# Optimization experiments

Measured on AMD Instinct MI355X. Metric: run time of the kernel, lower is better.

## Reference

```python
import jax, jax.numpy as jnp
import numpy as np


def setup_inputs() -> dict:
    key = jax.random.key(0)
    ks = jax.random.split(key, 6)
    B, D, U = 65536, 256, 256
    L, T, Ep, Es = 2, 2, 2, 2
    s = 1.0 / np.sqrt(D)  # VarianceScaling-like scale
    return {
        "x": jax.random.normal(ks[0], (B, D), jnp.float32),
        "we_task": jax.random.normal(ks[1], (L, T * Ep, D, U), jnp.float32) * s,
        "be_task": jnp.zeros((L, T * Ep, U), jnp.float32),
        "we_share": jax.random.normal(ks[2], (L, Es, D, U), jnp.float32) * s,
        "be_share": jnp.zeros((L, Es, U), jnp.float32),
        "wg_task": jax.random.normal(ks[3], (L, T, D, Ep + Es), jnp.float32) * s,
        "bg_task": jnp.zeros((L, T, Ep + Es), jnp.float32),
        "wg_share": jax.random.normal(ks[4], (L - 1, D, T * Ep + Es), jnp.float32) * s,
        "bg_share": jnp.zeros((L - 1, T * Ep + Es), jnp.float32),
    }


def reference(x, we_task, be_task, we_share, be_share, wg_task, bg_task, wg_share, bg_share):
    L, TE, D, U = we_task.shape
    T = wg_task.shape[1]
    Ep = TE // T
    Es = we_share.shape[1]
    B = x.shape[0]
    # PLE: level 0 feeds the same input to every task slot and the shared slot
    ins = [x] * (T + 1)
    for lvl in range(L):
        last = lvl == L - 1
        xt = jnp.stack(ins[:T])  # [T,B,D] task-specific inputs
        wt = we_task[lvl].reshape(T, Ep, D, U)
        bt = be_task[lvl].reshape(T, Ep, U)
        # task experts, batched over tasks and experts: [T,B,Ep,U]
        e_task = jax.nn.relu(jnp.einsum('tbd,tedu->tbeu', xt, wt) + bt[:, None, :, :])
        # shared experts on the shared input: [B,Es,U]
        e_share = jax.nn.relu(jnp.einsum('bd,edu->beu', ins[-1], we_share[lvl]) + be_share[lvl][None])
        # per-task softmax gates: [T,B,Ep+Es]
        gates = jax.nn.softmax(jnp.einsum('tbd,tdg->tbg', xt, wg_task[lvl]) + bg_task[lvl][:, None, :], axis=-1)
        outs = []
        for t in range(T):
            experts = jnp.concatenate([e_task[t], e_share], axis=1)  # [B,Ep+Es,U]
            outs.append(jnp.einsum('beu,be->bu', experts, gates[t]))
        if not last:
            g_s = jax.nn.softmax(ins[-1] @ wg_share[lvl] + bg_share[lvl], axis=-1)  # [B,T*Ep+Es]
            all_e = jnp.concatenate(
                [e_task.transpose(1, 0, 2, 3).reshape(B, T * Ep, U), e_share], axis=1)
            outs.append(jnp.einsum('beu,be->bu', all_e, g_s))
        ins = outs
    return jnp.stack(ins)  # [T,B,U]
```

## Files before the change

### kernel.cpp

```cpp
#include <hip/hip_runtime.h>

typedef short s8v __attribute__((ext_vector_type(8)));
typedef float f4v __attribute__((ext_vector_type(4)));

#define NB 65536
#define BT 64
#define STR 264
#define PW_ELEMS 786432
#define PG0_OFF  786432
#define PG1T0_OFF 790528
#define PG1T1_OFF 794624
#define TOTAL_PACK 798720

__device__ __forceinline__ unsigned short f2bf(float f) {
  unsigned u = __float_as_uint(f);
  u += 0x7FFF + ((u >> 16) & 1);
  return (unsigned short)(u >> 16);
}

__global__ void pack_weights(const float* __restrict__ we_task,
                             const float* __restrict__ we_share,
                             const float* __restrict__ wg_task,
                             const float* __restrict__ wg_share,
                             unsigned short* __restrict__ ws) {
  int i = blockIdx.x * 256 + threadIdx.x;
  if (i >= TOTAL_PACK) return;
  float v = 0.f;
  if (i < PW_ELEMS) {
    int j = i & 7;
    int t = i >> 3;
    int lane = t & 63; t >>= 6;
    int kc = t & 7;    t >>= 3;
    int nt = t & 15;   t >>= 4;
    int lvl = t / 6, e = t % 6;
    int d = kc * 32 + (lane >> 4) * 8 + j;
    int u = nt * 16 + (lane & 15);
    if (e < 4) v = we_task[((lvl * 4 + e) * 256 + d) * 256 + u];
    else       v = we_share[((lvl * 2 + (e - 4)) * 256 + d) * 256 + u];
  } else {
    int gi = i - PW_ELEMS;
    int which = gi >> 12;
    int r = gi & 4095;
    int j = r & 7;
    int lane = (r >> 3) & 63;
    int kc = r >> 9;
    int d = kc * 32 + (lane >> 4) * 8 + j;
    int n = lane & 15;
    if (which == 0) {
      if (n < 4)       v = wg_task[0 * 1024 + d * 4 + n];
      else if (n < 8)  v = wg_task[1 * 1024 + d * 4 + (n - 4)];
      else if (n < 14) v = wg_share[d * 6 + (n - 8)];
    } else if (which == 1) {
      if (n < 4) v = wg_task[2 * 1024 + d * 4 + n];
    } else {
      if (n < 4) v = wg_task[3 * 1024 + d * 4 + n];
    }
  }
  ws[i] = f2bf(v);
}

__device__ __forceinline__ s8v ld_af(const unsigned short* Ab, int m, int kc,
                                     int col, int rq) {
  return *(const s8v*)&Ab[(m * 16 + col) * STR + kc * 32 + rq * 8];
}

__launch_bounds__(512, 2)
__global__ void ple_fused(const float* __restrict__ x,
                          const float* __restrict__ be_task,
                          const float* __restrict__ be_share,
                          const float* __restrict__ bg_task,
                          const float* __restrict__ bg_share,
                          const unsigned short* __restrict__ ws,
                          float* __restrict__ out) {
  __shared__ unsigned short A0[BT * STR];
  __shared__ unsigned short A1[2][BT * STR];
  __shared__ unsigned short A2[BT * STR];
  __shared__ float g_lds[BT * 16];
  __shared__ float bias_lds[6 * 256];

  const int tid  = threadIdx.x;
  const int lane = tid & 63;
  const int wave = tid >> 6;
  const int col  = lane & 15;
  const int rq   = lane >> 4;
  const int r0   = blockIdx.x * BT;

  {
    const float* xb = x + (long)r0 * 256;
#pragma unroll
    for (int i = 0; i < 8; ++i) {
      int f = tid + i * 512;
      int row = f >> 6, c4 = f & 63;
      const float4 v = *(const float4*)(xb + row * 256 + c4 * 4);
      unsigned lo = ((unsigned)f2bf(v.y) << 16) | f2bf(v.x);
      unsigned hi = ((unsigned)f2bf(v.w) << 16) | f2bf(v.z);
      *(uint2*)&A0[row * STR + c4 * 4] = make_uint2(lo, hi);
    }
    for (int idx = tid; idx < 1536; idx += 512)
      bias_lds[idx] = (idx < 1024) ? be_task[idx] : be_share[idx - 1024];
  }
  __syncthreads();

  if (wave < 4) {
    const int m = wave;
    f4v ag = {0.f, 0.f, 0.f, 0.f};
    for (int kc = 0; kc < 8; ++kc) {
      s8v af = ld_af(A0, m, kc, col, rq);
      s8v bg = *(const s8v*)&ws[PG0_OFF + (kc * 64 + lane) * 8];
      ag = __builtin_amdgcn_mfma_f32_16x16x32_bf16(af, bg, ag, 0, 0, 0);
    }
#pragma unroll
    for (int r = 0; r < 4; ++r)
      g_lds[(m * 16 + rq * 4 + r) * 16 + col] = ag[r];
  }
  __syncthreads();

  if (tid < 64) {
    float* g = &g_lds[tid * 16];
    {
      float a0 = g[0] + bg_task[0], a1 = g[1] + bg_task[1];
      float a2 = g[2] + bg_task[2], a3 = g[3] + bg_task[3];
      float mx = fmaxf(fmaxf(a0, a1), fmaxf(a2, a3));
      float e0 = __expf(a0 - mx), e1 = __expf(a1 - mx);
      float e2 = __expf(a2 - mx), e3 = __expf(a3 - mx);
      float inv = 1.f / (e0 + e1 + e2 + e3);
      g[0] = e0 * inv; g[1] = e1 * inv; g[2] = e2 * inv; g[3] = e3 * inv;
    }
    {
      float a0 = g[4] + bg_task[4], a1 = g[5] + bg_task[5];
      float a2 = g[6] + bg_task[6], a3 = g[7] + bg_task[7];
      float mx = fmaxf(fmaxf(a0, a1), fmaxf(a2, a3));
      float e0 = __expf(a0 - mx), e1 = __expf(a1 - mx);
      float e2 = __expf(a2 - mx), e3 = __expf(a3 - mx);
      float inv = 1.f / (e0 + e1 + e2 + e3);
      g[4] = e0 * inv; g[5] = e1 * inv; g[6] = e2 * inv; g[7] = e3 * inv;
    }
    {
      float a[6], mx = -1e30f;
#pragma unroll
      for (int k = 0; k < 6; ++k) { a[k] = g[8 + k] + bg_share[k]; mx = fmaxf(mx, a[k]); }
      float s = 0.f;
#pragma unroll
      for (int k = 0; k < 6; ++k) { a[k] = __expf(a[k] - mx); s += a[k]; }
      float inv = 1.f / s;
#pragma unroll
      for (int k = 0; k < 6; ++k) g[8 + k] = a[k] * inv;
    }
  }
  __syncthreads();

#pragma unroll
  for (int q = 0; q < 2; ++q) {
    const int nt = wave + q * 8;
    f4v acc[4][6];
#pragma unroll
    for (int m = 0; m < 4; ++m)
#pragma unroll
      for (int e = 0; e < 6; ++e) acc[m][e] = (f4v){0.f, 0.f, 0.f, 0.f};

    const unsigned short* pw = ws + nt * 4096;
    s8v bfc[6];
#pragma unroll
    for (int e = 0; e < 6; ++e)
      bfc[e] = *(const s8v*)&pw[e * 65536 + lane * 8];
#pragma unroll
    for (int kc = 0; kc < 8; ++kc) {
      s8v bfn[6];
      if (kc < 7) {
#pragma unroll
        for (int e = 0; e < 6; ++e)
          bfn[e] = *(const s8v*)&pw[e * 65536 + ((kc + 1) * 64 + lane) * 8];
      }
      s8v af[4];
#pragma unroll
      for (int m = 0; m < 4; ++m) af[m] = ld_af(A0, m, kc, col, rq);
#pragma unroll
      for (int m = 0; m < 4; ++m)
#pragma unroll
        for (int e = 0; e < 6; ++e)
          acc[m][e] = __builtin_amdgcn_mfma_f32_16x16x32_bf16(af[m], bfc[e], acc[m][e], 0, 0, 0);
#pragma unroll
      for (int e = 0; e < 6; ++e) bfc[e] = bfn[e];
    }

    const int u = nt * 16 + col;
    float bz[6];
#pragma unroll
    for (int e = 0; e < 6; ++e) bz[e] = bias_lds[e * 256 + u];
#pragma unroll
    for (int m = 0; m < 4; ++m) {
#pragma unroll
      for (int r = 0; r < 4; ++r) {
        int row = m * 16 + rq * 4 + r;
        const float* gr = &g_lds[row * 16];
        f4v ga = *(const f4v*)&gr[0];
        f4v gb = *(const f4v*)&gr[4];
        f4v gc = *(const f4v*)&gr[8];
        float gs4 = gr[12], gs5 = gr[13];
        float E0 = fmaxf(acc[m][0][r] + bz[0], 0.f);
        float E1 = fmaxf(acc[m][1][r] + bz[1], 0.f);
        float E2 = fmaxf(acc[m][2][r] + bz[2], 0.f);
        float E3 = fmaxf(acc[m][3][r] + bz[3], 0.f);
        float E4 = fmaxf(acc[m][4][r] + bz[4], 0.f);
        float E5 = fmaxf(acc[m][5][r] + bz[5], 0.f);
        float o0 = ga[0] * E0 + ga[1] * E1 + ga[2] * E4 + ga[3] * E5;
        float o1 = gb[0] * E2 + gb[1] * E3 + gb[2] * E4 + gb[3] * E5;
        float o2 = gc[0] * E0 + gc[1] * E1 + gc[2] * E2 + gc[3] * E3 + gs4 * E4 + gs5 * E5;
        A1[0][row * STR + u] = f2bf(o0);
        A1[1][row * STR + u] = f2bf(o1);
        A2[row * STR + u]    = f2bf(o2);
      }
    }
  }
  __syncthreads();

  for (int idx = tid; idx < 1536; idx += 512)
    bias_lds[idx] = (idx < 1024) ? be_task[1024 + idx] : be_share[512 + idx - 1024];

  {
    const int m = wave >> 1;
    const int t = wave & 1;
    const unsigned short* pg = ws + (t ? PG1T1_OFF : PG1T0_OFF);
    f4v ag = {0.f, 0.f, 0.f, 0.f};
    for (int kc = 0; kc < 8; ++kc) {
      s8v af = ld_af(A1[t], m, kc, col, rq);
      s8v bg = *(const s8v*)&pg[(kc * 64 + lane) * 8];
      ag = __builtin_amdgcn_mfma_f32_16x16x32_bf16(af, bg, ag, 0, 0, 0);
    }
    if (col < 4) {
#pragma unroll
      for (int r = 0; r < 4; ++r)
        g_lds[(m * 16 + rq * 4 + r) * 16 + t * 4 + col] = ag[r];
    }
  }
  __syncthreads();

  if (tid < 64) {
    float* g = &g_lds[tid * 16];
    {
      float a0 = g[0] + bg_task[8],  a1 = g[1] + bg_task[9];
      float a2 = g[2] + bg_task[10], a3 = g[3] + bg_task[11];
      float mx = fmaxf(fmaxf(a0, a1), fmaxf(a2, a3));
      float e0 = __expf(a0 - mx), e1 = __expf(a1 - mx);
      float e2 = __expf(a2 - mx), e3 = __expf(a3 - mx);
      float inv = 1.f / (e0 + e1 + e2 + e3);
      g[0] = e0 * inv; g[1] = e1 * inv; g[2] = e2 * inv; g[3] = e3 * inv;
    }
    {
      float a0 = g[4] + bg_task[12], a1 = g[5] + bg_task[13];
      float a2 = g[6] + bg_task[14], a3 = g[7] + bg_task[15];
      float mx = fmaxf(fmaxf(a0, a1), fmaxf(a2, a3));
      float e0 = __expf(a0 - mx), e1 = __expf(a1 - mx);
      float e2 = __expf(a2 - mx), e3 = __expf(a3 - mx);
      float inv = 1.f / (e0 + e1 + e2 + e3);
      g[4] = e0 * inv; g[5] = e1 * inv; g[6] = e2 * inv; g[7] = e3 * inv;
    }
  }
  __syncthreads();

#pragma unroll
  for (int q = 0; q < 2; ++q) {
    const int nt = wave + q * 8;
    f4v acc[4][6];
#pragma unroll
    for (int m = 0; m < 4; ++m)
#pragma unroll
      for (int e = 0; e < 6; ++e) acc[m][e] = (f4v){0.f, 0.f, 0.f, 0.f};

    const unsigned short* pw = ws + 6 * 65536 + nt * 4096;
    s8v bfc[6];
#pragma unroll
    for (int e = 0; e < 6; ++e)
      bfc[e] = *(const s8v*)&pw[e * 65536 + lane * 8];
#pragma unroll
    for (int kc = 0; kc < 8; ++kc) {
      s8v bfn[6];
      if (kc < 7) {
#pragma unroll
        for (int e = 0; e < 6; ++e)
          bfn[e] = *(const s8v*)&pw[e * 65536 + ((kc + 1) * 64 + lane) * 8];
      }
      s8v a0f[4], a1f[4], a2f[4];
#pragma unroll
      for (int m = 0; m < 4; ++m) {
        a0f[m] = ld_af(A1[0], m, kc, col, rq);
        a1f[m] = ld_af(A1[1], m, kc, col, rq);
        a2f[m] = ld_af(A2,    m, kc, col, rq);
      }
#pragma unroll
      for (int m = 0; m < 4; ++m) {
        acc[m][0] = __builtin_amdgcn_mfma_f32_16x16x32_bf16(a0f[m], bfc[0], acc[m][0], 0, 0, 0);
        acc[m][1] = __builtin_amdgcn_mfma_f32_16x16x32_bf16(a0f[m], bfc[1], acc[m][1], 0, 0, 0);
        acc[m][2] = __builtin_amdgcn_mfma_f32_16x16x32_bf16(a1f[m], bfc[2], acc[m][2], 0, 0, 0);
        acc[m][3] = __builtin_amdgcn_mfma_f32_16x16x32_bf16(a1f[m], bfc[3], acc[m][3], 0, 0, 0);
        acc[m][4] = __builtin_amdgcn_mfma_f32_16x16x32_bf16(a2f[m], bfc[4], acc[m][4], 0, 0, 0);
        acc[m][5] = __builtin_amdgcn_mfma_f32_16x16x32_bf16(a2f[m], bfc[5], acc[m][5], 0, 0, 0);
      }
#pragma unroll
      for (int e = 0; e < 6; ++e) bfc[e] = bfn[e];
    }

    const int u = nt * 16 + col;
    float bz[6];
#pragma unroll
    for (int e = 0; e < 6; ++e) bz[e] = bias_lds[e * 256 + u];
#pragma unroll
    for (int m = 0; m < 4; ++m) {
#pragma unroll
      for (int r = 0; r < 4; ++r) {
        int row = m * 16 + rq * 4 + r;
        const float* gr = &g_lds[row * 16];
        f4v ga = *(const f4v*)&gr[0];
        f4v gb = *(const f4v*)&gr[4];
        float E0 = fmaxf(acc[m][0][r] + bz[0], 0.f);
        float E1 = fmaxf(acc[m][1][r] + bz[1], 0.f);
        float E2 = fmaxf(acc[m][2][r] + bz[2], 0.f);
        float E3 = fmaxf(acc[m][3][r] + bz[3], 0.f);
        float E4 = fmaxf(acc[m][4][r] + bz[4], 0.f);
        float E5 = fmaxf(acc[m][5][r] + bz[5], 0.f);
        float o0 = ga[0] * E0 + ga[1] * E1 + ga[2] * E4 + ga[3] * E5;
        float o1 = gb[0] * E2 + gb[1] * E3 + gb[2] * E4 + gb[3] * E5;
        out[(long)(r0 + row) * 256 + u] = o0;
        out[16777216L + (long)(r0 + row) * 256 + u] = o1;
      }
    }
  }
}

extern "C" void kernel_launch(void* const* d_in, const int* in_sizes, int n_in,
                              void* d_out, int out_size, void* d_ws, size_t ws_size,
                              hipStream_t stream) {
  const float* x        = (const float*)d_in[0];
  const float* we_task  = (const float*)d_in[1];
  const float* be_task  = (const float*)d_in[2];
  const float* we_share = (const float*)d_in[3];
  const float* be_share = (const float*)d_in[4];
  const float* wg_task  = (const float*)d_in[5];
  const float* bg_task  = (const float*)d_in[6];
  const float* wg_share = (const float*)d_in[7];
  const float* bg_share = (const float*)d_in[8];
  unsigned short* ws = (unsigned short*)d_ws;
  float* out = (float*)d_out;

  hipLaunchKernelGGL(pack_weights, dim3((TOTAL_PACK + 255) / 256), dim3(256), 0, stream,
                     we_task, we_share, wg_task, wg_share, ws);
  hipLaunchKernelGGL(ple_fused, dim3(NB / BT), dim3(512), 0, stream,
                     x, be_task, be_share, bg_task, bg_share, ws, out);
}
```

Measured before the change: 369.2 us.

## Switch expert GEMMs to 32x32x16 MFMA with repacked weight layout

```diff
diff --git a/kernel.cpp b/kernel.cpp
--- a/kernel.cpp
+++ b/kernel.cpp
@@ -2,6 +2,7 @@
 
 typedef short s8v __attribute__((ext_vector_type(8)));
 typedef float f4v __attribute__((ext_vector_type(4)));
+typedef float f16v __attribute__((ext_vector_type(16)));
 
 #define NB 65536
 #define BT 64
@@ -30,11 +31,11 @@
     int j = i & 7;
     int t = i >> 3;
     int lane = t & 63; t >>= 6;
-    int kc = t & 7;    t >>= 3;
-    int nt = t & 15;   t >>= 4;
+    int ks = t & 15;   t >>= 4;
+    int nt = t & 7;    t >>= 3;
     int lvl = t / 6, e = t % 6;
-    int d = kc * 32 + (lane >> 4) * 8 + j;
-    int u = nt * 16 + (lane & 15);
+    int d = ks * 16 + (lane >> 5) * 8 + j;
+    int u = nt * 32 + (lane & 31);
     if (e < 4) v = we_task[((lvl * 4 + e) * 256 + d) * 256 + u];
     else       v = we_share[((lvl * 2 + (e - 4)) * 256 + d) * 256 + u];
   } else {
@@ -59,9 +60,14 @@
   ws[i] = f2bf(v);
 }
 
-__device__ __forceinline__ s8v ld_af(const unsigned short* Ab, int m, int kc,
-                                     int col, int rq) {
+__device__ __forceinline__ s8v ld_a16(const unsigned short* Ab, int m, int kc,
+                                      int col, int rq) {
   return *(const s8v*)&Ab[(m * 16 + col) * STR + kc * 32 + rq * 8];
+}
+
+__device__ __forceinline__ s8v ld_a32(const unsigned short* Ab, int m, int ks,
+                                      int lane) {
+  return *(const s8v*)&Ab[(m * 32 + (lane & 31)) * STR + ks * 16 + (lane >> 5) * 8];
 }
 
 __launch_bounds__(512, 2)
@@ -83,6 +89,7 @@
   const int wave = tid >> 6;
   const int col  = lane & 15;
   const int rq   = lane >> 4;
+  const int hi   = lane >> 5;
   const int r0   = blockIdx.x * BT;
 
   {
@@ -93,8 +100,8 @@
       int row = f >> 6, c4 = f & 63;
       const float4 v = *(const float4*)(xb + row * 256 + c4 * 4);
       unsigned lo = ((unsigned)f2bf(v.y) << 16) | f2bf(v.x);
-      unsigned hi = ((unsigned)f2bf(v.w) << 16) | f2bf(v.z);
-      *(uint2*)&A0[row * STR + c4 * 4] = make_uint2(lo, hi);
+      unsigned hi2 = ((unsigned)f2bf(v.w) << 16) | f2bf(v.z);
+      *(uint2*)&A0[row * STR + c4 * 4] = make_uint2(lo, hi2);
     }
     for (int idx = tid; idx < 1536; idx += 512)
       bias_lds[idx] = (idx < 1024) ? be_task[idx] : be_share[idx - 1024];
@@ -105,7 +112,7 @@
     const int m = wave;
     f4v ag = {0.f, 0.f, 0.f, 0.f};
     for (int kc = 0; kc < 8; ++kc) {
-      s8v af = ld_af(A0, m, kc, col, rq);
+      s8v af = ld_a16(A0, m, kc, col, rq);
       s8v bg = *(const s8v*)&ws[PG0_OFF + (kc * 64 + lane) * 8];
       ag = __builtin_amdgcn_mfma_f32_16x16x32_bf16(af, bg, ag, 0, 0, 0);
     }
@@ -149,60 +156,53 @@
   }
   __syncthreads();
 
-#pragma unroll
-  for (int q = 0; q < 2; ++q) {
-    const int nt = wave + q * 8;
-    f4v acc[4][6];
-#pragma unroll
-    for (int m = 0; m < 4; ++m)
-#pragma unroll
-      for (int e = 0; e < 6; ++e) acc[m][e] = (f4v){0.f, 0.f, 0.f, 0.f};
-
-    const unsigned short* pw = ws + nt * 4096;
-    s8v bfc[6];
-#pragma unroll
-    for (int e = 0; e < 6; ++e)
-      bfc[e] = *(const s8v*)&pw[e * 65536 + lane * 8];
-#pragma unroll
-    for (int kc = 0; kc < 8; ++kc) {
-      s8v bfn[6];
-      if (kc < 7) {
+  {
+    const int nt = wave;
+    const int u  = nt * 32 + (lane & 31);
+    float bz[6];
+#pragma unroll
+    for (int e = 0; e < 6; ++e) bz[e] = bias_lds[e * 256 + u];
+
+#pragma unroll
+    for (int mp = 0; mp < 2; ++mp) {
+      f16v acc[6];
+#pragma unroll
+      for (int e = 0; e < 6; ++e) acc[e] = (f16v)(0.f);
+
+      s8v bfc[6];
+#pragma unroll
+      for (int e = 0; e < 6; ++e)
+        bfc[e] = *(const s8v*)&ws[(((e << 3) + nt) << 13) + lane * 8];
+#pragma unroll
+      for (int ks = 0; ks < 16; ++ks) {
+        s8v bfn[6];
+        if (ks < 15) {
+#pragma unroll
+          for (int e = 0; e < 6; ++e)
+            bfn[e] = *(const s8v*)&ws[(((e << 3) + nt) << 13) + (ks + 1) * 512 + lane * 8];
+        }
+        s8v af = ld_a32(A0, mp, ks, lane);
 #pragma unroll
         for (int e = 0; e < 6; ++e)
-          bfn[e] = *(const s8v*)&pw[e * 65536 + ((kc + 1) * 64 + lane) * 8];
+          acc[e] = __builtin_amdgcn_mfma_f32_32x32x16_bf16(af, bfc[e], acc[e], 0, 0, 0);
+#pragma unroll
+        for (int e = 0; e < 6; ++e) bfc[e] = bfn[e];
       }
-      s8v af[4];
-#pragma unroll
-      for (int m = 0; m < 4; ++m) af[m] = ld_af(A0, m, kc, col, rq);
-#pragma unroll
-      for (int m = 0; m < 4; ++m)
-#pragma unroll
-        for (int e = 0; e < 6; ++e)
-          acc[m][e] = __builtin_amdgcn_mfma_f32_16x16x32_bf16(af[m], bfc[e], acc[m][e], 0, 0, 0);
-#pragma unroll
-      for (int e = 0; e < 6; ++e) bfc[e] = bfn[e];
-    }
-
-    const int u = nt * 16 + col;
-    float bz[6];
-#pragma unroll
-    for (int e = 0; e < 6; ++e) bz[e] = bias_lds[e * 256 + u];
-#pragma unroll
-    for (int m = 0; m < 4; ++m) {
-#pragma unroll
-      for (int r = 0; r < 4; ++r) {
-        int row = m * 16 + rq * 4 + r;
+
+#pragma unroll
+      for (int r = 0; r < 16; ++r) {
+        int row = mp * 32 + (r & 3) + 8 * (r >> 2) + 4 * hi;
         const float* gr = &g_lds[row * 16];
         f4v ga = *(const f4v*)&gr[0];
         f4v gb = *(const f4v*)&gr[4];
         f4v gc = *(const f4v*)&gr[8];
         float gs4 = gr[12], gs5 = gr[13];
-        float E0 = fmaxf(acc[m][0][r] + bz[0], 0.f);
-        float E1 = fmaxf(acc[m][1][r] + bz[1], 0.f);
-        float E2 = fmaxf(acc[m][2][r] + bz[2], 0.f);
-        float E3 = fmaxf(acc[m][3][r] + bz[3], 0.f);
-        float E4 = fmaxf(acc[m][4][r] + bz[4], 0.f);
-        float E5 = fmaxf(acc[m][5][r] + bz[5], 0.f);
+        float E0 = fmaxf(acc[0][r] + bz[0], 0.f);
+        float E1 = fmaxf(acc[1][r] + bz[1], 0.f);
+        float E2 = fmaxf(acc[2][r] + bz[2], 0.f);
+        float E3 = fmaxf(acc[3][r] + bz[3], 0.f);
+        float E4 = fmaxf(acc[4][r] + bz[4], 0.f);
+        float E5 = fmaxf(acc[5][r] + bz[5], 0.f);
         float o0 = ga[0] * E0 + ga[1] * E1 + ga[2] * E4 + ga[3] * E5;
         float o1 = gb[0] * E2 + gb[1] * E3 + gb[2] * E4 + gb[3] * E5;
         float o2 = gc[0] * E0 + gc[1] * E1 + gc[2] * E2 + gc[3] * E3 + gs4 * E4 + gs5 * E5;
@@ -223,7 +223,7 @@
     const unsigned short* pg = ws + (t ? PG1T1_OFF : PG1T0_OFF);
     f4v ag = {0.f, 0.f, 0.f, 0.f};
     for (int kc = 0; kc < 8; ++kc) {
-      s8v af = ld_af(A1[t], m, kc, col, rq);
+      s8v af = ld_a16(A1[t], m, kc, col, rq);
       s8v bg = *(const s8v*)&pg[(kc * 64 + lane) * 8];
       ag = __builtin_amdgcn_mfma_f32_16x16x32_bf16(af, bg, ag, 0, 0, 0);
     }
@@ -258,66 +258,57 @@
   }
   __syncthreads();
 
-#pragma unroll
-  for (int q = 0; q < 2; ++q) {
-    const int nt = wave + q * 8;
-    f4v acc[4][6];
-#pragma unroll
-    for (int m = 0; m < 4; ++m)
-#pragma unroll
-      for (int e = 0; e < 6; ++e) acc[m][e] = (f4v){0.f, 0.f, 0.f, 0.f};
-
-    const unsigned short* pw = ws + 6 * 65536 + nt * 4096;
-    s8v bfc[6];
-#pragma unroll
-    for (int e = 0; e < 6; ++e)
-      bfc[e] = *(const s8v*)&pw[e * 65536 + lane * 8];
-#pragma unroll
-    for (int kc = 0; kc < 8; ++kc) {
-      s8v bfn[6];
-      if (kc < 7) {
-#pragma unroll
-        for (int e = 0; e < 6; ++e)
-          bfn[e] = *(const s8v*)&pw[e * 65536 + ((kc + 1) * 64 + lane) * 8];
+  {
+    const int nt = wave;
+    const int u  = nt * 32 + (lane & 31);
+    float bz[6];
+#pragma unroll
+    for (int e = 0; e < 6; ++e) bz[e] = bias_lds[e * 256 + u];
+
+#pragma unroll
+    for (int mp = 0; mp < 2; ++mp) {
+      f16v acc[6];
+#pragma unroll
+      for (int e = 0; e < 6; ++e) acc[e] = (f16v)(0.f);
+
+      const int l1b = 6 * 8 * 8192;
+      s8v bfc[6];
+#pragma unroll
+      for (int e = 0; e < 6; ++e)
+        bfc[e] = *(const s8v*)&ws[l1b + (((e << 3) + nt) << 13) + lane * 8];
+#pragma unroll
+      for (int ks = 0; ks < 16; ++ks) {
+        s8v bfn[6];
+        if (ks < 15) {
+#pragma unroll
+          for (int e = 0; e < 6; ++e)
+            bfn[e] = *(const s8v*)&ws[l1b + (((e << 3) + nt) << 13) + (ks + 1) * 512 + lane * 8];
+        }
+        s8v a0f = ld_a32(A1[0], mp, ks, lane);
+        s8v a1f = ld_a32(A1[1], mp, ks, lane);
+        s8v a2f = ld_a32(A2,    mp, ks, lane);
+        acc[0] = __builtin_amdgcn_mfma_f32_32x32x16_bf16(a0f, bfc[0], acc[0], 0, 0, 0);
+        acc[1] = __builtin_amdgcn_mfma_f32_32x32x16_bf16(a0f, bfc[1], acc[1], 0, 0, 0);
+        acc[2] = __builtin_amdgcn_mfma_f32_32x32x16_bf16(a1f, bfc[2], acc[2], 0, 0, 0);
+        acc[3] = __builtin_amdgcn_mfma_f32_32x32x16_bf16(a1f, bfc[3], acc[3], 0, 0, 0);
+        acc[4] = __builtin_amdgcn_mfma_f32_32x32x16_bf16(a2f, bfc[4], acc[4], 0, 0, 0);
+        acc[5] = __builtin_amdgcn_mfma_f32_32x32x16_bf16(a2f, bfc[5], acc[5], 0, 0, 0);
+#pragma unroll
+        for (int e = 0; e < 6; ++e) bfc[e] = bfn[e];
       }
-      s8v a0f[4], a1f[4], a2f[4];
-#pragma unroll
-      for (int m = 0; m < 4; ++m) {
-        a0f[m] = ld_af(A1[0], m, kc, col, rq);
-        a1f[m] = ld_af(A1[1], m, kc, col, rq);
-        a2f[m] = ld_af(A2,    m, kc, col, rq);
-      }
-#pragma unroll
-      for (int m = 0; m < 4; ++m) {
-        acc[m][0] = __builtin_amdgcn_mfma_f32_16x16x32_bf16(a0f[m], bfc[0], acc[m][0], 0, 0, 0);
-        acc[m][1] = __builtin_amdgcn_mfma_f32_16x16x32_bf16(a0f[m], bfc[1], acc[m][1], 0, 0, 0);
-        acc[m][2] = __builtin_amdgcn_mfma_f32_16x16x32_bf16(a1f[m], bfc[2], acc[m][2], 0, 0, 0);
-        acc[m][3] = __builtin_amdgcn_mfma_f32_16x16x32_bf16(a1f[m], bfc[3], acc[m][3], 0, 0, 0);
-        acc[m][4] = __builtin_amdgcn_mfma_f32_16x16x32_bf16(a2f[m], bfc[4], acc[m][4], 0, 0, 0);
-        acc[m][5] = __builtin_amdgcn_mfma_f32_16x16x32_bf16(a2f[m], bfc[5], acc[m][5], 0, 0, 0);
-      }
-#pragma unroll
-      for (int e = 0; e < 6; ++e) bfc[e] = bfn[e];
-    }
-
-    const int u = nt * 16 + col;
-    float bz[6];
-#pragma unroll
-    for (int e = 0; e < 6; ++e) bz[e] = bias_lds[e * 256 + u];
-#pragma unroll
-    for (int m = 0; m < 4; ++m) {
-#pragma unroll
-      for (int r = 0; r < 4; ++r) {
-        int row = m * 16 + rq * 4 + r;
+
+#pragma unroll
+      for (int r = 0; r < 16; ++r) {
+        int row = mp * 32 + (r & 3) + 8 * (r >> 2) + 4 * hi;
         const float* gr = &g_lds[row * 16];
         f4v ga = *(const f4v*)&gr[0];
         f4v gb = *(const f4v*)&gr[4];
-        float E0 = fmaxf(acc[m][0][r] + bz[0], 0.f);
-        float E1 = fmaxf(acc[m][1][r] + bz[1], 0.f);
-        float E2 = fmaxf(acc[m][2][r] + bz[2], 0.f);
-        float E3 = fmaxf(acc[m][3][r] + bz[3], 0.f);
-        float E4 = fmaxf(acc[m][4][r] + bz[4], 0.f);
-        float E5 = fmaxf(acc[m][5][r] + bz[5], 0.f);
+        float E0 = fmaxf(acc[0][r] + bz[0], 0.f);
+        float E1 = fmaxf(acc[1][r] + bz[1], 0.f);
+        float E2 = fmaxf(acc[2][r] + bz[2], 0.f);
+        float E3 = fmaxf(acc[3][r] + bz[3], 0.f);
+        float E4 = fmaxf(acc[4][r] + bz[4], 0.f);
+        float E5 = fmaxf(acc[5][r] + bz[5], 0.f);
         float o0 = ga[0] * E0 + ga[1] * E1 + ga[2] * E4 + ga[3] * E5;
         float o1 = gb[0] * E2 + gb[1] * E3 + gb[2] * E4 + gb[3] * E5;
         out[(long)(r0 + row) * 256 + u] = o0;
```

Result: faster. 326.0 us (-11.7%).
